# Optimization experiments

Hardware: AMD Instinct MI355X
Metric: run time of the kernel (lower is better)

The kernel has to match this reference:

```python
import jax, jax.numpy as jnp
import numpy as np

N_NODES = 50000


def setup_inputs() -> dict:
    key = jax.random.key(0)
    k1, k2, k3, k4, k5 = jax.random.split(key, 5)
    N, E, F_IN, F_E, F_OUT = N_NODES, 800000, 256, 64, 256
    feat = jax.random.normal(k1, (N, F_IN), dtype=jnp.float32)
    edge_feat = jax.random.normal(k2, (E, F_E), dtype=jnp.float32)
    # glorot-scaled weight for (in_feats+edge_feats, out_feats)
    limit = float(np.sqrt(6.0 / (F_IN + F_E + F_OUT)))
    weight = jax.random.uniform(k3, (F_IN + F_E, F_OUT), minval=-limit, maxval=limit, dtype=jnp.float32)
    bias = jnp.zeros((F_OUT,), dtype=jnp.float32)
    src = jax.random.randint(k4, (E,), 0, N, dtype=jnp.int32)
    dst = jax.random.randint(k5, (E,), 0, N, dtype=jnp.int32)
    return {"feat": feat, "edge_feat": edge_feat, "weight": weight, "bias": bias, "src": src, "dst": dst}


def reference(feat, edge_feat, weight, bias, src, dst):
    N, F_IN = feat.shape
    ones = jnp.ones(src.shape[0], dtype=jnp.float32)
    # out-degree normalization on source features
    out_deg = jax.ops.segment_sum(ones, src, num_segments=N)
    norm_out = jnp.maximum(out_deg, 1.0) ** -0.5  # [N]
    feat_n = feat * norm_out[:, None]
    # message = concat(feat_n[src], edge_feat); sum-aggregate by dst.
    # No activation on messages (double_activation=False), so sum distributes
    # over the concat halves -> two segment sums, identical math.
    agg_h = jax.ops.segment_sum(feat_n[src], dst, num_segments=N)      # [N, F_IN]
    agg_e = jax.ops.segment_sum(edge_feat, dst, num_segments=N)        # [N, F_E]
    rst = jnp.concatenate([agg_h, agg_e], axis=1) @ weight             # [N, F_OUT]
    # in-degree normalization on destination
    in_deg = jax.ops.segment_sum(ones, dst, num_segments=N)
    norm_in = jnp.maximum(in_deg, 1.0) ** -0.5
    rst = rst * norm_in[:, None] + bias
    return jax.nn.relu(rst)
```

## Files before the change

kernel.cpp:

```cpp
#include <hip/hip_runtime.h>

#define FIN 256
#define FE  64
#define FOUT 256
#define KTOT 320

typedef __attribute__((ext_vector_type(8))) short short8;
typedef __attribute__((ext_vector_type(4))) float f32x4;

__device__ inline unsigned short f2bf(float f) {
    unsigned int u = __builtin_bit_cast(unsigned int, f);
    u += 0x7fffu + ((u >> 16) & 1u);
    return (unsigned short)(u >> 16);
}
__device__ inline float bfu(unsigned short b) {
    return __builtin_bit_cast(float, (unsigned int)b << 16);
}


__global__ void k_deg_prepw(const int* __restrict__ src, const int* __restrict__ dst,
                            int* __restrict__ out_deg, int* __restrict__ in_deg,
                            const float* __restrict__ w, unsigned short* __restrict__ wtt,
                            int E) {
    int i = blockIdx.x * blockDim.x + threadIdx.x;
    if (i < E) {
        atomicAdd(&out_deg[src[i]], 1);
        atomicAdd(&in_deg[dst[i]], 1);
    }
    if (i < KTOT * 256) {
        int k = i >> 8, n = i & 255;
        wtt[n * KTOT + k] = f2bf(w[i]);
    }
}


__global__ __launch_bounds__(1024) void k_scan(const int* __restrict__ in_deg,
                                               const int* __restrict__ out_deg,
                                               int* __restrict__ row_ptr,
                                               int* __restrict__ cursor,
                                               float* __restrict__ norm_out,
                                               float* __restrict__ norm_in, int N) {
    __shared__ int red[16];
    __shared__ int wsum[16];
    __shared__ int wo[17];
    int b = blockIdx.x, t = threadIdx.x;
    int lane = t & 63, w = t >> 6;
    int limit = b << 10;

    int part = 0;
    for (int i = t; i < limit; i += 1024) part += in_deg[i];
#pragma unroll
    for (int off = 32; off; off >>= 1) part += __shfl_down(part, off, 64);
    if (lane == 0) red[w] = part;
    __syncthreads();
    if (t == 0) {
        int s = 0;
#pragma unroll
        for (int k = 0; k < 16; k++) s += red[k];
        red[0] = s;
    }
    __syncthreads();
    int base = red[0];

    int i = limit + t;
    int v = (i < N) ? in_deg[i] : 0;
    int incl = v;
#pragma unroll
    for (int off = 1; off < 64; off <<= 1) {
        int x = __shfl_up(incl, off, 64);
        if (lane >= off) incl += x;
    }
    if (lane == 63) wsum[w] = incl;
    __syncthreads();
    if (w == 0 && lane < 16) {
        int s = wsum[lane];
        int sc = s;
#pragma unroll
        for (int off = 1; off < 16; off <<= 1) {
            int x = __shfl_up(sc, off, 64);
            if (lane >= off) sc += x;
        }
        wo[lane] = sc - s;
        if (lane == 15) wo[16] = sc;
    }
    __syncthreads();
    int excl = base + wo[w] + incl - v;
    if (i < N) {
        row_ptr[i] = excl;
        cursor[i] = excl;
        norm_in[i]  = 1.0f / sqrtf((float)max(v, 1));
        norm_out[i] = 1.0f / sqrtf((float)max(out_deg[i], 1));
    }
    if (t == 0 && i + 1024 > N && i < N + 1024) row_ptr[N] = base + wo[16];
}


__global__ void k_scatter_prepf(const int* __restrict__ src, const int* __restrict__ dst,
                                int* __restrict__ cursor, int2* __restrict__ s_se, int E,
                                const float* __restrict__ feat,
                                const float* __restrict__ norm_out,
                                unsigned short* __restrict__ featb, int N) {
    int i = blockIdx.x * blockDim.x + threadIdx.x;
    if (i < E) {
        int d = dst[i];
        int p = atomicAdd(&cursor[d], 1);
        s_se[p] = make_int2(src[i], i);
    }
    if (i < N * 64) {
        int m = i >> 6, c4 = (i & 63) * 4;
        float s = norm_out[m];
        float4 v = *(const float4*)&feat[(size_t)m * FIN + c4];
        ushort4 o;
        o.x = f2bf(v.x * s); o.y = f2bf(v.y * s); o.z = f2bf(v.z * s); o.w = f2bf(v.w * s);
        *(ushort4*)&featb[(size_t)m * FIN + c4] = o;
    }
}


__global__ __launch_bounds__(256) void k_agg(const unsigned short* __restrict__ featb,
                                             const float* __restrict__ edge_feat,
                                             const int* __restrict__ row_ptr,
                                             const int2* __restrict__ s_se,
                                             unsigned short* __restrict__ aggb, int N) {
    int t = threadIdx.x;
    int w = t >> 6, lane = t & 63;
    int n = blockIdx.x * 4 + w;
    if (n >= N) return;

    int beg = row_ptr[n], end = row_ptr[n + 1];
    float h0 = 0.f, h1 = 0.f, h2 = 0.f, h3 = 0.f, eacc = 0.f;
    int p = beg;

    for (; p + 8 <= end; p += 8) {
        int2 i0 = s_se[p + 0], i1 = s_se[p + 1], i2 = s_se[p + 2], i3 = s_se[p + 3];
        int2 i4 = s_se[p + 4], i5 = s_se[p + 5], i6 = s_se[p + 6], i7 = s_se[p + 7];
        ushort4 f0 = *(const ushort4*)&featb[(size_t)i0.x * FIN + lane * 4];
        ushort4 f1 = *(const ushort4*)&featb[(size_t)i1.x * FIN + lane * 4];
        ushort4 f2 = *(const ushort4*)&featb[(size_t)i2.x * FIN + lane * 4];
        ushort4 f3 = *(const ushort4*)&featb[(size_t)i3.x * FIN + lane * 4];
        ushort4 f4 = *(const ushort4*)&featb[(size_t)i4.x * FIN + lane * 4];
        ushort4 f5 = *(const ushort4*)&featb[(size_t)i5.x * FIN + lane * 4];
        ushort4 f6 = *(const ushort4*)&featb[(size_t)i6.x * FIN + lane * 4];
        ushort4 f7 = *(const ushort4*)&featb[(size_t)i7.x * FIN + lane * 4];
        float e0 = __builtin_nontemporal_load(&edge_feat[(size_t)i0.y * FE + lane]);
        float e1 = __builtin_nontemporal_load(&edge_feat[(size_t)i1.y * FE + lane]);
        float e2 = __builtin_nontemporal_load(&edge_feat[(size_t)i2.y * FE + lane]);
        float e3 = __builtin_nontemporal_load(&edge_feat[(size_t)i3.y * FE + lane]);
        float e4 = __builtin_nontemporal_load(&edge_feat[(size_t)i4.y * FE + lane]);
        float e5 = __builtin_nontemporal_load(&edge_feat[(size_t)i5.y * FE + lane]);
        float e6 = __builtin_nontemporal_load(&edge_feat[(size_t)i6.y * FE + lane]);
        float e7 = __builtin_nontemporal_load(&edge_feat[(size_t)i7.y * FE + lane]);
        h0 += ((bfu(f0.x) + bfu(f1.x)) + (bfu(f2.x) + bfu(f3.x))) +
              ((bfu(f4.x) + bfu(f5.x)) + (bfu(f6.x) + bfu(f7.x)));
        h1 += ((bfu(f0.y) + bfu(f1.y)) + (bfu(f2.y) + bfu(f3.y))) +
              ((bfu(f4.y) + bfu(f5.y)) + (bfu(f6.y) + bfu(f7.y)));
        h2 += ((bfu(f0.z) + bfu(f1.z)) + (bfu(f2.z) + bfu(f3.z))) +
              ((bfu(f4.z) + bfu(f5.z)) + (bfu(f6.z) + bfu(f7.z)));
        h3 += ((bfu(f0.w) + bfu(f1.w)) + (bfu(f2.w) + bfu(f3.w))) +
              ((bfu(f4.w) + bfu(f5.w)) + (bfu(f6.w) + bfu(f7.w)));
        eacc += ((e0 + e1) + (e2 + e3)) + ((e4 + e5) + (e6 + e7));
    }
    if (p + 4 <= end) {
        int2 i0 = s_se[p + 0], i1 = s_se[p + 1], i2 = s_se[p + 2], i3 = s_se[p + 3];
        ushort4 f0 = *(const ushort4*)&featb[(size_t)i0.x * FIN + lane * 4];
        ushort4 f1 = *(const ushort4*)&featb[(size_t)i1.x * FIN + lane * 4];
        ushort4 f2 = *(const ushort4*)&featb[(size_t)i2.x * FIN + lane * 4];
        ushort4 f3 = *(const ushort4*)&featb[(size_t)i3.x * FIN + lane * 4];
        float e0 = __builtin_nontemporal_load(&edge_feat[(size_t)i0.y * FE + lane]);
        float e1 = __builtin_nontemporal_load(&edge_feat[(size_t)i1.y * FE + lane]);
        float e2 = __builtin_nontemporal_load(&edge_feat[(size_t)i2.y * FE + lane]);
        float e3 = __builtin_nontemporal_load(&edge_feat[(size_t)i3.y * FE + lane]);
        h0 += (bfu(f0.x) + bfu(f1.x)) + (bfu(f2.x) + bfu(f3.x));
        h1 += (bfu(f0.y) + bfu(f1.y)) + (bfu(f2.y) + bfu(f3.y));
        h2 += (bfu(f0.z) + bfu(f1.z)) + (bfu(f2.z) + bfu(f3.z));
        h3 += (bfu(f0.w) + bfu(f1.w)) + (bfu(f2.w) + bfu(f3.w));
        eacc += (e0 + e1) + (e2 + e3);
        p += 4;
    }
    for (; p < end; p++) {
        int2 a = s_se[p];
        ushort4 f0 = *(const ushort4*)&featb[(size_t)a.x * FIN + lane * 4];
        h0 += bfu(f0.x); h1 += bfu(f0.y); h2 += bfu(f0.z); h3 += bfu(f0.w);
        eacc += __builtin_nontemporal_load(&edge_feat[(size_t)a.y * FE + lane]);
    }

    ushort4 o;
    o.x = f2bf(h0); o.y = f2bf(h1); o.z = f2bf(h2); o.w = f2bf(h3);
    *(ushort4*)&aggb[(size_t)n * KTOT + lane * 4] = o;
    aggb[(size_t)n * KTOT + FIN + lane] = f2bf(eacc);
}


#define GTM 128
#define GBK 64
#define ALD 72

__global__ __launch_bounds__(256) void k_gemm_fused(const unsigned short* __restrict__ A,
                                                    int M,
                                                    const unsigned short* __restrict__ Wt,
                                                    const float* __restrict__ norm_in,
                                                    const float* __restrict__ bias,
                                                    float* __restrict__ out) {
    __shared__ unsigned short As[GTM * ALD];
    __shared__ unsigned short Bs[GTM * ALD];
    int m0 = blockIdx.y * GTM;
    int n0 = blockIdx.x * GTM;
    int t = threadIdx.x;
    int wave = t >> 6, lane = t & 63;
    int wy = wave >> 1, wx = wave & 1;
    int quad = lane >> 4, l16 = lane & 15;

    f32x4 acc[4][4];
#pragma unroll
    for (int i = 0; i < 4; i++)
#pragma unroll
        for (int j = 0; j < 4; j++) acc[i][j] = (f32x4){0.f, 0.f, 0.f, 0.f};

    for (int k0 = 0; k0 < KTOT; k0 += GBK) {
#pragma unroll
        for (int q = 0; q < 4; q++) {
            int idx = t + q * 256;
            int row = idx >> 3;
            int c16 = idx & 7;
            int gm = m0 + row;
            uint4 v = make_uint4(0, 0, 0, 0);
            if (gm < M) v = *(const uint4*)&A[(size_t)gm * KTOT + k0 + c16 * 8];
            *(uint4*)&As[row * ALD + c16 * 8] = v;
        }
#pragma unroll
        for (int q = 0; q < 4; q++) {
            int idx = t + q * 256;
            int row = idx >> 3;
            int c16 = idx & 7;
            uint4 v = *(const uint4*)&Wt[(size_t)(n0 + row) * KTOT + k0 + c16 * 8];
            *(uint4*)&Bs[row * ALD + c16 * 8] = v;
        }
        __syncthreads();
#pragma unroll
        for (int kk = 0; kk < GBK / 32; kk++) {
            short8 af[4], bf[4];
#pragma unroll
            for (int i = 0; i < 4; i++) {
                af[i] = *(const short8*)&As[(wy * 64 + i * 16 + l16) * ALD + kk * 32 + quad * 8];
                bf[i] = *(const short8*)&Bs[(wx * 64 + i * 16 + l16) * ALD + kk * 32 + quad * 8];
            }
#pragma unroll
            for (int i = 0; i < 4; i++)
#pragma unroll
                for (int j = 0; j < 4; j++)
                    acc[i][j] = __builtin_amdgcn_mfma_f32_16x16x32_bf16(af[i], bf[j], acc[i][j], 0, 0, 0);
        }
        __syncthreads();
    }

#pragma unroll
    for (int i = 0; i < 4; i++)
#pragma unroll
        for (int r = 0; r < 4; r++) {
            int gm = m0 + wy * 64 + i * 16 + quad * 4 + r;
            if (gm < M) {
                float ni = norm_in[gm];
#pragma unroll
                for (int j = 0; j < 4; j++) {
                    int gn = n0 + wx * 64 + j * 16 + l16;
                    float v = fmaxf(acc[i][j][r] * ni + bias[gn], 0.f);
                    out[(size_t)gm * FOUT + gn] = v;
                }
            }
        }
}


extern "C" void kernel_launch(void* const* d_in, const int* in_sizes, int n_in,
                              void* d_out, int out_size, void* d_ws, size_t ws_size,
                              hipStream_t stream) {
    const float* feat      = (const float*)d_in[0];
    const float* edge_feat = (const float*)d_in[1];
    const float* weight    = (const float*)d_in[2];
    const float* bias      = (const float*)d_in[3];
    const int*   src       = (const int*)d_in[4];
    const int*   dst       = (const int*)d_in[5];
    int E = in_sizes[4];
    int N = in_sizes[0] / FIN;

    char* ws = (char*)d_ws;
    size_t off = 0;
    auto alloc = [&](size_t bytes) -> void* {
        void* p = ws + off;
        off += (bytes + 255) & ~(size_t)255;
        return p;
    };
    unsigned short* featb = (unsigned short*)alloc((size_t)N * FIN * 2);
    unsigned short* aggb  = (unsigned short*)alloc((size_t)N * KTOT * 2);
    unsigned short* wtt   = (unsigned short*)alloc((size_t)256 * KTOT * 2);
    int*   out_deg  = (int*)alloc((size_t)2 * N * 4);
    int*   in_deg   = out_deg + N;
    int*   row_ptr  = (int*)alloc((size_t)(N + 1) * 4);
    int*   cursor   = (int*)alloc((size_t)N * 4);
    float* norm_out = (float*)alloc((size_t)N * 4);
    float* norm_in  = (float*)alloc((size_t)N * 4);
    int2*  s_se     = (int2*)alloc((size_t)E * 8);
    (void)ws_size;

    int bE = (E + 255) / 256;
    int nchunk = (N + 1023) >> 10;

    hipMemsetAsync(out_deg, 0, (size_t)2 * N * 4, stream);

    k_deg_prepw<<<bE, 256, 0, stream>>>(src, dst, out_deg, in_deg, weight, wtt, E);
    k_scan<<<nchunk, 1024, 0, stream>>>(in_deg, out_deg, row_ptr, cursor,
                                        norm_out, norm_in, N);
    k_scatter_prepf<<<(N * 64 + 255) / 256, 256, 0, stream>>>(src, dst, cursor, s_se, E,
                                                              feat, norm_out, featb, N);

    k_agg<<<(N + 3) / 4, 256, 0, stream>>>(featb, edge_feat, row_ptr, s_se, aggb, N);

    dim3 gg(FOUT / GTM, (N + GTM - 1) / GTM);
    k_gemm_fused<<<gg, 256, 0, stream>>>(aggb, N, wtt, norm_in, bias, (float*)d_out);
}
```

Baseline: 500.0 us.

## Fuse neighbor aggregation into GEMM via shared-memory A tile

Merges the gather/aggregation kernel and the GEMM: each block aggregates 64 destination rows directly into a full-K shared-memory A tile, then multiplies against all 256 output columns of the bf16 weight. This removes the aggb global write/read round trip and one launch. In exchange each block serializes 16 rows per wave of irregular gathers before MFMA work, with fewer concurrent waves in flight for latency hiding, and the weight tile is reloaded per block.

Result: slower. 558.0 us (+11.6%).

```diff
diff --git a/kernel.cpp b/kernel.cpp
--- a/kernel.cpp
+++ b/kernel.cpp
@@ -117,98 +117,92 @@
 }
 
 
-__global__ __launch_bounds__(256) void k_agg(const unsigned short* __restrict__ featb,
-                                             const float* __restrict__ edge_feat,
-                                             const int* __restrict__ row_ptr,
-                                             const int2* __restrict__ s_se,
-                                             unsigned short* __restrict__ aggb, int N) {
+#define GTM  64
+#define AKLD 328
+#define BKLD 72
+
+__global__ __launch_bounds__(256) void k_agg_gemm(const unsigned short* __restrict__ featb,
+                                                  const float* __restrict__ edge_feat,
+                                                  const int* __restrict__ row_ptr,
+                                                  const int2* __restrict__ s_se,
+                                                  const unsigned short* __restrict__ Wt,
+                                                  const float* __restrict__ norm_in,
+                                                  const float* __restrict__ bias,
+                                                  float* __restrict__ out, int N) {
+    __shared__ unsigned short As[GTM * AKLD];
+    __shared__ unsigned short Bs[256 * BKLD];
     int t = threadIdx.x;
     int w = t >> 6, lane = t & 63;
-    int n = blockIdx.x * 4 + w;
-    if (n >= N) return;
-
-    int beg = row_ptr[n], end = row_ptr[n + 1];
-    float h0 = 0.f, h1 = 0.f, h2 = 0.f, h3 = 0.f, eacc = 0.f;
-    int p = beg;
-
-    for (; p + 8 <= end; p += 8) {
-        int2 i0 = s_se[p + 0], i1 = s_se[p + 1], i2 = s_se[p + 2], i3 = s_se[p + 3];
-        int2 i4 = s_se[p + 4], i5 = s_se[p + 5], i6 = s_se[p + 6], i7 = s_se[p + 7];
-        ushort4 f0 = *(const ushort4*)&featb[(size_t)i0.x * FIN + lane * 4];
-        ushort4 f1 = *(const ushort4*)&featb[(size_t)i1.x * FIN + lane * 4];
-        ushort4 f2 = *(const ushort4*)&featb[(size_t)i2.x * FIN + lane * 4];
-        ushort4 f3 = *(const ushort4*)&featb[(size_t)i3.x * FIN + lane * 4];
-        ushort4 f4 = *(const ushort4*)&featb[(size_t)i4.x * FIN + lane * 4];
-        ushort4 f5 = *(const ushort4*)&featb[(size_t)i5.x * FIN + lane * 4];
-        ushort4 f6 = *(const ushort4*)&featb[(size_t)i6.x * FIN + lane * 4];
-        ushort4 f7 = *(const ushort4*)&featb[(size_t)i7.x * FIN + lane * 4];
-        float e0 = __builtin_nontemporal_load(&edge_feat[(size_t)i0.y * FE + lane]);
-        float e1 = __builtin_nontemporal_load(&edge_feat[(size_t)i1.y * FE + lane]);
-        float e2 = __builtin_nontemporal_load(&edge_feat[(size_t)i2.y * FE + lane]);
-        float e3 = __builtin_nontemporal_load(&edge_feat[(size_t)i3.y * FE + lane]);
-        float e4 = __builtin_nontemporal_load(&edge_feat[(size_t)i4.y * FE + lane]);
-        float e5 = __builtin_nontemporal_load(&edge_feat[(size_t)i5.y * FE + lane]);
-        float e6 = __builtin_nontemporal_load(&edge_feat[(size_t)i6.y * FE + lane]);
-        float e7 = __builtin_nontemporal_load(&edge_feat[(size_t)i7.y * FE + lane]);
-        h0 += ((bfu(f0.x) + bfu(f1.x)) + (bfu(f2.x) + bfu(f3.x))) +
-              ((bfu(f4.x) + bfu(f5.x)) + (bfu(f6.x) + bfu(f7.x)));
-        h1 += ((bfu(f0.y) + bfu(f1.y)) + (bfu(f2.y) + bfu(f3.y))) +
-              ((bfu(f4.y) + bfu(f5.y)) + (bfu(f6.y) + bfu(f7.y)));
-        h2 += ((bfu(f0.z) + bfu(f1.z)) + (bfu(f2.z) + bfu(f3.z))) +
-              ((bfu(f4.z) + bfu(f5.z)) + (bfu(f6.z) + bfu(f7.z)));
-        h3 += ((bfu(f0.w) + bfu(f1.w)) + (bfu(f2.w) + bfu(f3.w))) +
-              ((bfu(f4.w) + bfu(f5.w)) + (bfu(f6.w) + bfu(f7.w)));
-        eacc += ((e0 + e1) + (e2 + e3)) + ((e4 + e5) + (e6 + e7));
-    }
-    if (p + 4 <= end) {
-        int2 i0 = s_se[p + 0], i1 = s_se[p + 1], i2 = s_se[p + 2], i3 = s_se[p + 3];
-        ushort4 f0 = *(const ushort4*)&featb[(size_t)i0.x * FIN + lane * 4];
-        ushort4 f1 = *(const ushort4*)&featb[(size_t)i1.x * FIN + lane * 4];
-        ushort4 f2 = *(const ushort4*)&featb[(size_t)i2.x * FIN + lane * 4];
-        ushort4 f3 = *(const ushort4*)&featb[(size_t)i3.x * FIN + lane * 4];
-        float e0 = __builtin_nontemporal_load(&edge_feat[(size_t)i0.y * FE + lane]);
-        float e1 = __builtin_nontemporal_load(&edge_feat[(size_t)i1.y * FE + lane]);
-        float e2 = __builtin_nontemporal_load(&edge_feat[(size_t)i2.y * FE + lane]);
-        float e3 = __builtin_nontemporal_load(&edge_feat[(size_t)i3.y * FE + lane]);
-        h0 += (bfu(f0.x) + bfu(f1.x)) + (bfu(f2.x) + bfu(f3.x));
-        h1 += (bfu(f0.y) + bfu(f1.y)) + (bfu(f2.y) + bfu(f3.y));
-        h2 += (bfu(f0.z) + bfu(f1.z)) + (bfu(f2.z) + bfu(f3.z));
-        h3 += (bfu(f0.w) + bfu(f1.w)) + (bfu(f2.w) + bfu(f3.w));
-        eacc += (e0 + e1) + (e2 + e3);
-        p += 4;
-    }
-    for (; p < end; p++) {
-        int2 a = s_se[p];
-        ushort4 f0 = *(const ushort4*)&featb[(size_t)a.x * FIN + lane * 4];
-        h0 += bfu(f0.x); h1 += bfu(f0.y); h2 += bfu(f0.z); h3 += bfu(f0.w);
-        eacc += __builtin_nontemporal_load(&edge_feat[(size_t)a.y * FE + lane]);
-    }
-
-    ushort4 o;
-    o.x = f2bf(h0); o.y = f2bf(h1); o.z = f2bf(h2); o.w = f2bf(h3);
-    *(ushort4*)&aggb[(size_t)n * KTOT + lane * 4] = o;
-    aggb[(size_t)n * KTOT + FIN + lane] = f2bf(eacc);
-}
-
-
-#define GTM 128
-#define GBK 64
-#define ALD 72
-
-__global__ __launch_bounds__(256) void k_gemm_fused(const unsigned short* __restrict__ A,
-                                                    int M,
-                                                    const unsigned short* __restrict__ Wt,
-                                                    const float* __restrict__ norm_in,
-                                                    const float* __restrict__ bias,
-                                                    float* __restrict__ out) {
-    __shared__ unsigned short As[GTM * ALD];
-    __shared__ unsigned short Bs[GTM * ALD];
-    int m0 = blockIdx.y * GTM;
-    int n0 = blockIdx.x * GTM;
-    int t = threadIdx.x;
-    int wave = t >> 6, lane = t & 63;
-    int wy = wave >> 1, wx = wave & 1;
     int quad = lane >> 4, l16 = lane & 15;
+    int m0 = blockIdx.x * GTM;
+
+#pragma unroll 1
+    for (int i = 0; i < 16; i++) {
+        int row = w * 16 + i;
+        int n = m0 + row;
+        float h0 = 0.f, h1 = 0.f, h2 = 0.f, h3 = 0.f, eacc = 0.f;
+        if (n < N) {
+            int beg = row_ptr[n], end = row_ptr[n + 1];
+            int p = beg;
+            for (; p + 8 <= end; p += 8) {
+                int2 i0 = s_se[p + 0], i1 = s_se[p + 1], i2 = s_se[p + 2], i3 = s_se[p + 3];
+                int2 i4 = s_se[p + 4], i5 = s_se[p + 5], i6 = s_se[p + 6], i7 = s_se[p + 7];
+                ushort4 f0 = *(const ushort4*)&featb[(size_t)i0.x * FIN + lane * 4];
+                ushort4 f1 = *(const ushort4*)&featb[(size_t)i1.x * FIN + lane * 4];
+                ushort4 f2 = *(const ushort4*)&featb[(size_t)i2.x * FIN + lane * 4];
+                ushort4 f3 = *(const ushort4*)&featb[(size_t)i3.x * FIN + lane * 4];
+                ushort4 f4 = *(const ushort4*)&featb[(size_t)i4.x * FIN + lane * 4];
+                ushort4 f5 = *(const ushort4*)&featb[(size_t)i5.x * FIN + lane * 4];
+                ushort4 f6 = *(const ushort4*)&featb[(size_t)i6.x * FIN + lane * 4];
+                ushort4 f7 = *(const ushort4*)&featb[(size_t)i7.x * FIN + lane * 4];
+                float e0 = __builtin_nontemporal_load(&edge_feat[(size_t)i0.y * FE + lane]);
+                float e1 = __builtin_nontemporal_load(&edge_feat[(size_t)i1.y * FE + lane]);
+                float e2 = __builtin_nontemporal_load(&edge_feat[(size_t)i2.y * FE + lane]);
+                float e3 = __builtin_nontemporal_load(&edge_feat[(size_t)i3.y * FE + lane]);
+                float e4 = __builtin_nontemporal_load(&edge_feat[(size_t)i4.y * FE + lane]);
+                float e5 = __builtin_nontemporal_load(&edge_feat[(size_t)i5.y * FE + lane]);
+                float e6 = __builtin_nontemporal_load(&edge_feat[(size_t)i6.y * FE + lane]);
+                float e7 = __builtin_nontemporal_load(&edge_feat[(size_t)i7.y * FE + lane]);
+                h0 += ((bfu(f0.x) + bfu(f1.x)) + (bfu(f2.x) + bfu(f3.x))) +
+                      ((bfu(f4.x) + bfu(f5.x)) + (bfu(f6.x) + bfu(f7.x)));
+                h1 += ((bfu(f0.y) + bfu(f1.y)) + (bfu(f2.y) + bfu(f3.y))) +
+                      ((bfu(f4.y) + bfu(f5.y)) + (bfu(f6.y) + bfu(f7.y)));
+                h2 += ((bfu(f0.z) + bfu(f1.z)) + (bfu(f2.z) + bfu(f3.z))) +
+                      ((bfu(f4.z) + bfu(f5.z)) + (bfu(f6.z) + bfu(f7.z)));
+                h3 += ((bfu(f0.w) + bfu(f1.w)) + (bfu(f2.w) + bfu(f3.w))) +
+                      ((bfu(f4.w) + bfu(f5.w)) + (bfu(f6.w) + bfu(f7.w)));
+                eacc += ((e0 + e1) + (e2 + e3)) + ((e4 + e5) + (e6 + e7));
+            }
+            if (p + 4 <= end) {
+                int2 i0 = s_se[p + 0], i1 = s_se[p + 1], i2 = s_se[p + 2], i3 = s_se[p + 3];
+                ushort4 f0 = *(const ushort4*)&featb[(size_t)i0.x * FIN + lane * 4];
+                ushort4 f1 = *(const ushort4*)&featb[(size_t)i1.x * FIN + lane * 4];
+                ushort4 f2 = *(const ushort4*)&featb[(size_t)i2.x * FIN + lane * 4];
+                ushort4 f3 = *(const ushort4*)&featb[(size_t)i3.x * FIN + lane * 4];
+                float e0 = __builtin_nontemporal_load(&edge_feat[(size_t)i0.y * FE + lane]);
+                float e1 = __builtin_nontemporal_load(&edge_feat[(size_t)i1.y * FE + lane]);
+                float e2 = __builtin_nontemporal_load(&edge_feat[(size_t)i2.y * FE + lane]);
+                float e3 = __builtin_nontemporal_load(&edge_feat[(size_t)i3.y * FE + lane]);
+                h0 += (bfu(f0.x) + bfu(f1.x)) + (bfu(f2.x) + bfu(f3.x));
+                h1 += (bfu(f0.y) + bfu(f1.y)) + (bfu(f2.y) + bfu(f3.y));
+                h2 += (bfu(f0.z) + bfu(f1.z)) + (bfu(f2.z) + bfu(f3.z));
+                h3 += (bfu(f0.w) + bfu(f1.w)) + (bfu(f2.w) + bfu(f3.w));
+                eacc += (e0 + e1) + (e2 + e3);
+                p += 4;
+            }
+            for (; p < end; p++) {
+                int2 a = s_se[p];
+                ushort4 f0 = *(const ushort4*)&featb[(size_t)a.x * FIN + lane * 4];
+                h0 += bfu(f0.x); h1 += bfu(f0.y); h2 += bfu(f0.z); h3 += bfu(f0.w);
+                eacc += __builtin_nontemporal_load(&edge_feat[(size_t)a.y * FE + lane]);
+            }
+        }
+        ushort4 o;
+        o.x = f2bf(h0); o.y = f2bf(h1); o.z = f2bf(h2); o.w = f2bf(h3);
+        *(ushort4*)&As[row * AKLD + lane * 4] = o;
+        As[row * AKLD + FIN + lane] = f2bf(eacc);
+    }
+    __syncthreads();
 
     f32x4 acc[4][4];
 #pragma unroll
@@ -216,39 +210,29 @@
 #pragma unroll
         for (int j = 0; j < 4; j++) acc[i][j] = (f32x4){0.f, 0.f, 0.f, 0.f};
 
-    for (int k0 = 0; k0 < KTOT; k0 += GBK) {
-#pragma unroll
-        for (int q = 0; q < 4; q++) {
+    for (int k0 = 0; k0 < KTOT; k0 += 64) {
+#pragma unroll
+        for (int q = 0; q < 8; q++) {
             int idx = t + q * 256;
             int row = idx >> 3;
             int c16 = idx & 7;
-            int gm = m0 + row;
-            uint4 v = make_uint4(0, 0, 0, 0);
-            if (gm < M) v = *(const uint4*)&A[(size_t)gm * KTOT + k0 + c16 * 8];
-            *(uint4*)&As[row * ALD + c16 * 8] = v;
-        }
-#pragma unroll
-        for (int q = 0; q < 4; q++) {
-            int idx = t + q * 256;
-            int row = idx >> 3;
-            int c16 = idx & 7;
-            uint4 v = *(const uint4*)&Wt[(size_t)(n0 + row) * KTOT + k0 + c16 * 8];
-            *(uint4*)&Bs[row * ALD + c16 * 8] = v;
+            uint4 v = *(const uint4*)&Wt[(size_t)row * KTOT + k0 + c16 * 8];
+            *(uint4*)&Bs[row * BKLD + c16 * 8] = v;
         }
         __syncthreads();
 #pragma unroll
-        for (int kk = 0; kk < GBK / 32; kk++) {
-            short8 af[4], bf[4];
+        for (int kk = 0; kk < 2; kk++) {
+            short8 af[4], bf4[4];
 #pragma unroll
             for (int i = 0; i < 4; i++) {
-                af[i] = *(const short8*)&As[(wy * 64 + i * 16 + l16) * ALD + kk * 32 + quad * 8];
-                bf[i] = *(const short8*)&Bs[(wx * 64 + i * 16 + l16) * ALD + kk * 32 + quad * 8];
+                af[i]  = *(const short8*)&As[(i * 16 + l16) * AKLD + k0 + kk * 32 + quad * 8];
+                bf4[i] = *(const short8*)&Bs[(w * 64 + i * 16 + l16) * BKLD + kk * 32 + quad * 8];
             }
 #pragma unroll
             for (int i = 0; i < 4; i++)
 #pragma unroll
                 for (int j = 0; j < 4; j++)
-                    acc[i][j] = __builtin_amdgcn_mfma_f32_16x16x32_bf16(af[i], bf[j], acc[i][j], 0, 0, 0);
+                    acc[i][j] = __builtin_amdgcn_mfma_f32_16x16x32_bf16(af[i], bf4[j], acc[i][j], 0, 0, 0);
         }
         __syncthreads();
     }
@@ -257,12 +241,12 @@
     for (int i = 0; i < 4; i++)
 #pragma unroll
         for (int r = 0; r < 4; r++) {
-            int gm = m0 + wy * 64 + i * 16 + quad * 4 + r;
-            if (gm < M) {
+            int gm = m0 + i * 16 + quad * 4 + r;
+            if (gm < N) {
                 float ni = norm_in[gm];
 #pragma unroll
                 for (int j = 0; j < 4; j++) {
-                    int gn = n0 + wx * 64 + j * 16 + l16;
+                    int gn = w * 64 + j * 16 + l16;
                     float v = fmaxf(acc[i][j][r] * ni + bias[gn], 0.f);
                     out[(size_t)gm * FOUT + gn] = v;
                 }
@@ -291,7 +275,6 @@
         return p;
     };
     unsigned short* featb = (unsigned short*)alloc((size_t)N * FIN * 2);
-    unsigned short* aggb  = (unsigned short*)alloc((size_t)N * KTOT * 2);
     unsigned short* wtt   = (unsigned short*)alloc((size_t)256 * KTOT * 2);
     int*   out_deg  = (int*)alloc((size_t)2 * N * 4);
     int*   in_deg   = out_deg + N;
@@ -313,8 +296,7 @@
     k_scatter_prepf<<<(N * 64 + 255) / 256, 256, 0, stream>>>(src, dst, cursor, s_se, E,
                                                               feat, norm_out, featb, N);
 
-    k_agg<<<(N + 3) / 4, 256, 0, stream>>>(featb, edge_feat, row_ptr, s_se, aggb, N);
-
-    dim3 gg(FOUT / GTM, (N + GTM - 1) / GTM);
-    k_gemm_fused<<<gg, 256, 0, stream>>>(aggb, N, wtt, norm_in, bias, (float*)d_out);
-}
+    k_agg_gemm<<<(N + GTM - 1) / GTM, 256, 0, stream>>>(featb, edge_feat, row_ptr, s_se,
+                                                        wtt, norm_in, bias,
+                                                        (float*)d_out, N);
+}
```
